# Kernel optimization log

Hardware: AMD Instinct MI355X
Metric: run time of the kernel (lower is better)

The kernel has to match this reference:

```python
import jax, jax.numpy as jnp
import numpy as np

DIM, HEADS = 1536, 12
HD = DIM // HEADS            # 128 head dim
C = HD // 2                  # 64 complex (pair) dim
C0 = C - 2 * (C // 3)        # 22 (temporal axis)
C1 = C // 3                  # 21 (each spatial axis)
MAX_POS = 1024
F_, H_, W_ = 9, 22, 22
SEQ = F_ * H_ * W_           # 4356
NCLASS = 2
EPS = 1e-6


def _rope_tables():
    # Wan rope_params: theta = 10000, per-axis half-dims C0, C1, C1.
    def ang(half):
        inv = 1.0 / (10000.0 ** (np.arange(0, 2 * half, 2) / (2 * half)))
        return np.outer(np.arange(MAX_POS), inv)
    a = np.concatenate([ang(C0), ang(C1), ang(C1)], axis=1)  # [MAX_POS, C]
    return jnp.asarray(np.cos(a), jnp.float32), jnp.asarray(np.sin(a), jnp.float32)


def setup_inputs() -> dict:
    key = jax.random.key(0)
    ks = jax.random.split(key, 6)
    s = 1.0 / np.sqrt(DIM)
    def lin(k):
        k1, k2 = jax.random.split(k)
        return (jax.random.uniform(k1, (DIM, DIM), jnp.float32, -s, s),
                jax.random.uniform(k2, (DIM,), jnp.float32, -s, s))
    Wq, bq = lin(ks[0]); Wk, bk = lin(ks[1]); Wv, bv = lin(ks[2]); Wo, bo = lin(ks[3])
    fc, fs = _rope_tables()
    masks = (jax.random.uniform(ks[4], (NCLASS, H_ * W_)) < 0.5).astype(jnp.float32)
    x = jax.random.normal(ks[5], (1, SEQ, DIM), jnp.float32)
    return {"x": x, "Wq": Wq, "bq": bq, "Wk": Wk, "bk": bk, "Wv": Wv, "bv": bv,
            "Wo": Wo, "bo": bo, "gq": jnp.ones((DIM,), jnp.float32),
            "gk": jnp.ones((DIM,), jnp.float32), "freqs_cos": fc, "freqs_sin": fs,
            "ref_target_masks": masks, "f": F_, "h": H_, "w": W_}


def _rmsnorm(x, g):
    return x * jax.lax.rsqrt(jnp.mean(x * x, axis=-1, keepdims=True) + EPS) * g


def _grid_cs(tab, f, h, w):
    # per-position (f,h,w) rope table -> [f*h*w, C]
    p0 = jnp.broadcast_to(tab[:f, None, None, :C0], (f, h, w, C0))
    p1 = jnp.broadcast_to(tab[None, :h, None, C0:C0 + C1], (f, h, w, C1))
    p2 = jnp.broadcast_to(tab[None, None, :w, C0 + C1:], (f, h, w, C1))
    return jnp.concatenate([p0, p1, p2], axis=-1).reshape(f * h * w, C)


def _rope(x, cos, sin):
    # x: [b,s,n,d]; pairs are interleaved along d (view_as_complex semantics)
    b, s, n, d = x.shape
    xr = x.reshape(b, s, n, d // 2, 2)
    a, bi = xr[..., 0], xr[..., 1]
    cos = cos[None, :, None, :]
    sin = sin[None, :, None, :]
    out = jnp.stack([a * cos - bi * sin, a * sin + bi * cos], axis=-1)
    return out.reshape(b, s, n, d)


def reference(x, Wq, bq, Wk, bk, Wv, bv, Wo, bo, gq, gk, freqs_cos, freqs_sin,
              ref_target_masks, f, h, w):
    b, s, _ = x.shape
    n, d = HEADS, HD
    q = _rmsnorm(x @ Wq.T + bq, gq).reshape(b, s, n, d)
    k = _rmsnorm(x @ Wk.T + bk, gk).reshape(b, s, n, d)
    v = (x @ Wv.T + bv).reshape(b, s, n, d)
    cos = _grid_cs(freqs_cos, f, h, w)
    sin = _grid_cs(freqs_sin, f, h, w)
    q = _rope(q, cos, sin)
    k = _rope(k, cos, sin)
    scale = 1.0 / np.sqrt(d).astype(np.float32)
    # full (window_size == (-1,-1)) attention; seq_lens == s so k_lens mask is identity
    scores = jnp.einsum('bsnd,btnd->bnst', q, k) * scale
    p = jax.nn.softmax(scores, axis=-1)
    o = jnp.einsum('bnst,btnd->bsnd', p, v).reshape(b, s, n * d)
    out = o @ Wo.T + bo
    # aux attention map vs reference-frame keys (first h*w spatial tokens), no-grad path
    xs = h * w
    ref_k = k[:, :xs]
    s2 = jnp.einsum('bsnd,btnd->bnst', q * scale, ref_k)
    p2 = jax.nn.softmax(s2, axis=-1)                       # [b,n,s,xs]
    m = ref_target_masks                                   # [c,xs]
    maps = jnp.einsum('bnst,ct->cbns', p2, m) / jnp.sum(m, axis=-1)[:, None, None, None]
    attn_map = maps.mean(axis=2).reshape(-1, s)            # mean over heads -> [c*b, s]
    return out, attn_map
```

## Files before the change

kernel.cpp:

```cpp
#include <hip/hip_runtime.h>
#include <hip/hip_bf16.h>
#include <math.h>

constexpr int SEQ   = 4356;
constexpr int DIM   = 1536;
constexpr int HEADS = 12;
constexpr int HD    = 128;
constexpr int CH    = 64;
constexpr int C0c   = 22;
constexpr int C1c   = 21;
constexpr int WWc   = 22;
constexpr int HHWW  = 484;
constexpr int XS    = 484;
constexpr int KVB   = 32;
constexpr int NT    = (SEQ + KVB - 1) / KVB;
constexpr int SEQP  = 4416;
constexpr int VP    = 40;
constexpr size_t SD = (size_t)SEQ * DIM;

typedef float f32x4 __attribute__((ext_vector_type(4)));
typedef short bf16x8 __attribute__((ext_vector_type(8)));
typedef short bf16x4 __attribute__((ext_vector_type(4)));

__device__ inline unsigned short f2bf(float f) {
  union { float f; unsigned u; } x; x.f = f;
  return (unsigned short)((x.u + 0x7FFFu + ((x.u >> 16) & 1u)) >> 16);
}

#define GLD16(g, l)                                                                        \
  __builtin_amdgcn_global_load_lds((const __attribute__((address_space(1))) unsigned*)    \
                                       (const void*)(g),                                  \
                                   (__attribute__((address_space(3))) unsigned*)(void*)(l),\
                                   16, 0, 0)

__global__ __launch_bounds__(256) void prep_kernel(const float* __restrict__ mask,
                                                   float* __restrict__ amap,
                                                   float* __restrict__ cnt,
                                                   float4* __restrict__ msk4) {
  int t = threadIdx.x;
  for (int i = t; i < 2 * SEQ; i += 256) amap[i] = 0.f;
  for (int i = t; i < 512; i += 256) {
    float4 v;
    v.x = (i < XS) ? mask[i] : 0.f;
    v.y = (i < XS) ? mask[XS + i] : 0.f;
    v.z = (i < XS) ? 1.f : 0.f;
    v.w = 0.f;
    msk4[i] = v;
  }
  float c0 = 0.f, c1 = 0.f;
  for (int i = t; i < XS; i += 256) { c0 += mask[i]; c1 += mask[XS + i]; }
  __shared__ float red0[256];
  __shared__ float red1[256];
  red0[t] = c0; red1[t] = c1;
  __syncthreads();
  for (int off = 128; off > 0; off >>= 1) {
    if (t < off) { red0[t] += red0[t + off]; red1[t] += red1[t + off]; }
    __syncthreads();
  }
  if (t == 0) { cnt[0] = red0[0]; cnt[1] = red1[0]; }
}

__global__ __launch_bounds__(256) void padzero(unsigned short* __restrict__ vt) {
  const int pad = SEQP - SEQ;
  const int total = DIM * pad;
  for (int i = blockIdx.x * 256 + threadIdx.x; i < total; i += gridDim.x * 256) {
    const int d = i / pad, c = i - d * pad;
    vt[(size_t)d * SEQP + SEQ + c] = 0;
  }
}

__global__ __launch_bounds__(256) void to_bf16(const float* __restrict__ in,
                                               unsigned short* __restrict__ out, int n4) {
  for (int i = blockIdx.x * 256 + threadIdx.x; i < n4; i += gridDim.x * 256) {
    const float4 v = ((const float4*)in)[i];
    ushort4 o;
    o.x = f2bf(v.x); o.y = f2bf(v.y); o.z = f2bf(v.z); o.w = f2bf(v.w);
    ((ushort4*)out)[i] = o;
  }
}

__global__ __launch_bounds__(256) void to_bf16_w(const float* __restrict__ W0, const float* __restrict__ W1,
                                                 const float* __restrict__ W2, const float* __restrict__ W3,
                                                 unsigned short* __restrict__ o0, unsigned short* __restrict__ o1,
                                                 unsigned short* __restrict__ o2, unsigned short* __restrict__ o3,
                                                 int n4) {
  const int z = blockIdx.z;
  const float* in = (z == 0) ? W0 : (z == 1) ? W1 : (z == 2) ? W2 : W3;
  unsigned short* out = (z == 0) ? o0 : (z == 1) ? o1 : (z == 2) ? o2 : o3;
  for (int i = blockIdx.x * 256 + threadIdx.x; i < n4; i += gridDim.x * 256) {
    const float4 v = ((const float4*)in)[i];
    ushort4 o;
    o.x = f2bf(v.x); o.y = f2bf(v.y); o.z = f2bf(v.z); o.w = f2bf(v.w);
    ((ushort4*)out)[i] = o;
  }
}

__global__ __launch_bounds__(256) void gemm_qkv(const unsigned short* __restrict__ A,
                                                const unsigned short* __restrict__ B0,
                                                const unsigned short* __restrict__ B1,
                                                const unsigned short* __restrict__ B2,
                                                const float* __restrict__ bq,
                                                const float* __restrict__ bk,
                                                const float* __restrict__ bv,
                                                float* __restrict__ o0,
                                                float* __restrict__ o1,
                                                unsigned short* __restrict__ vtout,
                                                int M) {
  __shared__ unsigned short As[128 * 64];
  __shared__ unsigned short Bs[128 * 64];
  const int z = blockIdx.z;
  const unsigned short* B = (z == 0) ? B0 : (z == 1) ? B1 : B2;
  const float* bias = (z == 0) ? bq : (z == 1) ? bk : bv;
  const int t    = threadIdx.x;
  const int lane = t & 63;
  const int w    = t >> 6;
  const int wr   = w >> 1, wc = w & 1;
  const int bm = blockIdx.x * 128, bn = blockIdx.y * 128;
  const int lq = lane & 15, lg = lane >> 4;
  f32x4 acc[4][4] = {};
  for (int k0 = 0; k0 < DIM; k0 += 64) {
#pragma unroll
    for (int i = 0; i < 4; ++i) {
      const int idx = i * 256 + t;
      const int row = idx >> 3;
      const int c8  = (idx & 7) * 8;
      const int ga  = min(bm + row, M - 1);
      GLD16(A + (size_t)ga * DIM + k0 + c8, As + idx * 8);
      const int gb  = bn + row;
      GLD16(B + (size_t)gb * DIM + k0 + c8, Bs + idx * 8);
    }
    __syncthreads();
#pragma unroll
    for (int kk = 0; kk < 2; ++kk) {
      bf16x8 af[4], bf[4];
#pragma unroll
      for (int m = 0; m < 4; ++m)
        af[m] = *(const bf16x8*)(As + (wr * 64 + m * 16 + lq) * 64 + kk * 32 + lg * 8);
#pragma unroll
      for (int n = 0; n < 4; ++n)
        bf[n] = *(const bf16x8*)(Bs + (wc * 64 + n * 16 + lq) * 64 + kk * 32 + lg * 8);
#pragma unroll
      for (int m = 0; m < 4; ++m)
#pragma unroll
        for (int n = 0; n < 4; ++n)
          acc[m][n] = __builtin_amdgcn_mfma_f32_16x16x32_bf16(af[m], bf[n], acc[m][n], 0, 0, 0);
    }
    __syncthreads();
  }
#pragma unroll
  for (int n = 0; n < 4; ++n) {
    const int col = bn + wc * 64 + n * 16 + lq;
    const float bv2 = bias[col];
#pragma unroll
    for (int m = 0; m < 4; ++m) {
      const int rm = bm + wr * 64 + m * 16 + lg * 4;
      if (z < 2) {
        float* C = (z == 0) ? o0 : o1;
#pragma unroll
        for (int r = 0; r < 4; ++r) {
          const int row = rm + r;
          if (row < M) C[(size_t)row * DIM + col] = acc[m][n][r] + bv2;
        }
      } else {
        if (rm < M) {
          bf16x4 o;
#pragma unroll
          for (int r = 0; r < 4; ++r) o[r] = (short)f2bf(acc[m][n][r] + bv2);
          *(bf16x4*)(vtout + (size_t)col * SEQP + rm) = o;
        }
      }
    }
  }
}

__global__ __launch_bounds__(256) void gemm_mfma(const unsigned short* __restrict__ A,
                                                 const unsigned short* __restrict__ B,
                                                 const float* __restrict__ bias,
                                                 float* __restrict__ C, int M) {
  __shared__ unsigned short As[128 * 64];
  __shared__ unsigned short Bs[128 * 64];
  const int t    = threadIdx.x;
  const int lane = t & 63;
  const int w    = t >> 6;
  const int wr   = w >> 1, wc = w & 1;
  const int bm = blockIdx.x * 128, bn = blockIdx.y * 128;
  const int lq = lane & 15, lg = lane >> 4;
  f32x4 acc[4][4] = {};
  for (int k0 = 0; k0 < DIM; k0 += 64) {
#pragma unroll
    for (int i = 0; i < 4; ++i) {
      const int idx = i * 256 + t;
      const int row = idx >> 3;
      const int c8  = (idx & 7) * 8;
      const int ga  = min(bm + row, M - 1);
      GLD16(A + (size_t)ga * DIM + k0 + c8, As + idx * 8);
      const int gb  = bn + row;
      GLD16(B + (size_t)gb * DIM + k0 + c8, Bs + idx * 8);
    }
    __syncthreads();
#pragma unroll
    for (int kk = 0; kk < 2; ++kk) {
      bf16x8 af[4], bf[4];
#pragma unroll
      for (int m = 0; m < 4; ++m)
        af[m] = *(const bf16x8*)(As + (wr * 64 + m * 16 + lq) * 64 + kk * 32 + lg * 8);
#pragma unroll
      for (int n = 0; n < 4; ++n)
        bf[n] = *(const bf16x8*)(Bs + (wc * 64 + n * 16 + lq) * 64 + kk * 32 + lg * 8);
#pragma unroll
      for (int m = 0; m < 4; ++m)
#pragma unroll
        for (int n = 0; n < 4; ++n)
          acc[m][n] = __builtin_amdgcn_mfma_f32_16x16x32_bf16(af[m], bf[n], acc[m][n], 0, 0, 0);
    }
    __syncthreads();
  }
#pragma unroll
  for (int n = 0; n < 4; ++n) {
    const int col = bn + wc * 64 + n * 16 + lq;
    const float bv = bias[col];
#pragma unroll
    for (int m = 0; m < 4; ++m) {
      const int rm = bm + wr * 64 + m * 16 + lg * 4;
#pragma unroll
      for (int r = 0; r < 4; ++r) {
        const int row = rm + r;
        if (row < M) C[(size_t)row * DIM + col] = acc[m][n][r] + bv;
      }
    }
  }
}

__global__ __launch_bounds__(256) void rms_rope2(const float* __restrict__ qy,
                                                 const float* __restrict__ ky,
                                                 const float* __restrict__ gq,
                                                 const float* __restrict__ gk,
                                                 const float* __restrict__ fcos,
                                                 const float* __restrict__ fsin,
                                                 unsigned short* __restrict__ qout,
                                                 unsigned short* __restrict__ kout) {
  const int z = blockIdx.y;
  const float* y = z ? ky : qy;
  const float* g = z ? gk : gq;
  unsigned short* outb = z ? kout : qout;
  const float scale = z ? 1.0f : 0.08838834764831845f;
  const int s = blockIdx.x;
  const float* row = y + (size_t)s * DIM;
  const int t = threadIdx.x;
  float ss = 0.f;
  for (int i = t; i < DIM / 4; i += 256) {
    const float4 v = ((const float4*)row)[i];
    ss += v.x * v.x + v.y * v.y + v.z * v.z + v.w * v.w;
  }
#pragma unroll
  for (int off = 1; off < 64; off <<= 1) ss += __shfl_xor(ss, off);
  __shared__ float wred[4];
  if ((t & 63) == 0) wred[t >> 6] = ss;
  __syncthreads();
  const float tot = wred[0] + wred[1] + wred[2] + wred[3];
  const float rs = rsqrtf(tot * (1.0f / DIM) + 1e-6f);
  const int fi  = s / HHWW;
  const int rem = s - fi * HHWW;
  const int hi  = rem / WWc;
  const int wi  = rem - hi * WWc;
  for (int p = t; p < DIM / 2; p += 256) {
    const int head = p >> 6;
    const int c    = p & 63;
    const int idx  = head * HD + 2 * c;
    const int trow = (c < C0c) ? fi : ((c < C0c + C1c) ? hi : wi);
    const float co = fcos[trow * CH + c];
    const float si = fsin[trow * CH + c];
    const float a  = row[idx] * rs * g[idx];
    const float b  = row[idx + 1] * rs * g[idx + 1];
    ushort2 pr;
    pr.x = f2bf((a * co - b * si) * scale);
    pr.y = f2bf((a * si + b * co) * scale);
    *(ushort2*)(outb + (size_t)s * DIM + idx) = pr;
  }
}

#define TILE_BODY(KB_, MAP_, LAST_, PRE_)                                               \
  {                                                                                     \
    const int kb_ = (KB_);                                                              \
    f32x4 sacc[2] = {};                                                                 \
    _Pragma("unroll")                                                                   \
    for (int kbi = 0; kbi < 2; ++kbi) {                                                 \
      const int krow = kbi * 16 + lq;                                                   \
      _Pragma("unroll")                                                                 \
      for (int c = 0; c < 4; ++c) {                                                     \
        const bf16x8 kf = *(const bf16x8*)((char*)Ks + krow * 256 +                     \
                            (((c * 4 + lg) ^ (krow & 7)) * 16));                        \
        sacc[kbi] = __builtin_amdgcn_mfma_f32_16x16x32_bf16(kf, qf[c], sacc[kbi], 0, 0, 0); \
      }                                                                                 \
    }                                                                                   \
    if (PRE_) {                                                                         \
      const int kbn = kb_ + KVB;                                                        \
      _Pragma("unroll")                                                                 \
      for (int j = 0; j < 2; ++j) {                                                     \
        const int ck = t + j * 256;                                                     \
        const int kr = ck >> 4, ks2 = ck & 15;                                          \
        stK[j] = *(const bf16x8*)(kh + (size_t)min(kbn + kr, SEQ - 1) * DIM + ks2 * 8); \
        const int vd = ck >> 2, vs2 = ck & 3;                                           \
        stV[j] = *(const bf16x8*)(vh + (size_t)vd * SEQP + kbn + vs2 * 8);              \
      }                                                                                 \
    }                                                                                   \
    float sv[8];                                                                        \
    float mt = -1e30f;                                                                  \
    _Pragma("unroll")                                                                   \
    for (int i = 0; i < 8; ++i) {                                                       \
      float v = sacc[i >> 2][i & 3];                                                    \
      if (LAST_) {                                                                      \
        const int key = kb_ + (i >> 2) * 16 + lg * 4 + (i & 3);                         \
        if (key >= SEQ) v = -1e30f;                                                     \
      }                                                                                 \
      sv[i] = v;                                                                        \
      mt = fmaxf(mt, v);                                                                \
    }                                                                                   \
    mt = fmaxf(mt, __shfl_xor(mt, 16));                                                 \
    mt = fmaxf(mt, __shfl_xor(mt, 32));                                                 \
    const bool need = __any(mt > m_run + 8.f);                                          \
    if (need) {                                                                         \
      const float m_new = fmaxf(m_run, mt);                                             \
      const float alpha = __expf(m_run - m_new);                                        \
      m_run = m_new;                                                                    \
      l_run *= alpha;                                                                   \
      _Pragma("unroll")                                                                 \
      for (int db = 0; db < 8; ++db) {                                                  \
        acc[db][0] *= alpha; acc[db][1] *= alpha;                                       \
        acc[db][2] *= alpha; acc[db][3] *= alpha;                                       \
      }                                                                                 \
      if (MAP_) { d2 *= alpha; n0 *= alpha; n1 *= alpha; }                              \
    }                                                                                   \
    float ps = 0.f;                                                                     \
    _Pragma("unroll")                                                                   \
    for (int i = 0; i < 8; ++i) { sv[i] = __expf(sv[i] - m_run); ps += sv[i]; }         \
    ps += __shfl_xor(ps, 16);                                                           \
    ps += __shfl_xor(ps, 32);                                                           \
    l_run += ps;                                                                        \
    if (MAP_) {                                                                         \
      _Pragma("unroll")                                                                 \
      for (int i = 0; i < 8; ++i) {                                                     \
        const int key = kb_ + (i >> 2) * 16 + lg * 4 + (i & 3);                         \
        const float4 mv = Msk[key];                                                     \
        n0 = fmaf(sv[i], mv.x, n0);                                                     \
        n1 = fmaf(sv[i], mv.y, n1);                                                     \
        d2 = fmaf(sv[i], mv.z, d2);                                                     \
      }                                                                                 \
    }                                                                                   \
    _Pragma("unroll")                                                                   \
    for (int kbi = 0; kbi < 2; ++kbi) {                                                 \
      unsigned r0, r1;                                                                  \
      asm("v_cvt_pk_bf16_f32 %0, %1, %2" : "=v"(r0) : "v"(sv[kbi * 4 + 0]), "v"(sv[kbi * 4 + 1])); \
      asm("v_cvt_pk_bf16_f32 %0, %1, %2" : "=v"(r1) : "v"(sv[kbi * 4 + 2]), "v"(sv[kbi * 4 + 3])); \
      uint2 pw; pw.x = r0; pw.y = r1;                                                   \
      *(uint2*)&P[lq][kbi * 16 + lg * 4] = pw;                                          \
    }                                                                                   \
    {                                                                                   \
      const bf16x8 pf = *(const bf16x8*)&P[lq][lg * 8];                                 \
      _Pragma("unroll")                                                                 \
      for (int db = 0; db < 8; ++db) {                                                  \
        const bf16x8 vf = *(const bf16x8*)(Vs + (db * 16 + lq) * VP + lg * 8);          \
        acc[db] = __builtin_amdgcn_mfma_f32_16x16x32_bf16(vf, pf, acc[db], 0, 0, 0);    \
      }                                                                                 \
    }                                                                                   \
    if (PRE_) {                                                                         \
      __syncthreads();                                                                  \
      _Pragma("unroll")                                                                 \
      for (int j = 0; j < 2; ++j) {                                                     \
        const int ck = t + j * 256;                                                     \
        const int kr = ck >> 4, ks2 = ck & 15;                                          \
        *(bf16x8*)((char*)Ks + kr * 256 + ((ks2 ^ (kr & 7)) * 16)) = stK[j];            \
        const int vd = ck >> 2, vs2 = ck & 3;                                           \
        *(bf16x8*)(Vs + vd * VP + vs2 * 8) = stV[j];                                    \
      }                                                                                 \
      __syncthreads();                                                                  \
    }                                                                                   \
  }

__global__ __launch_bounds__(256, 4) void flash_mfma(const unsigned short* __restrict__ qbuf,
                                                     const unsigned short* __restrict__ kbuf,
                                                     const unsigned short* __restrict__ vt,
                                                     const float4* __restrict__ msk4,
                                                     const float* __restrict__ cnt,
                                                     unsigned short* __restrict__ ob,
                                                     float* __restrict__ amap) {
  const int h    = blockIdx.y;
  const int t    = threadIdx.x;
  const int w    = t >> 6;
  const int lane = t & 63;
  const int lq   = lane & 15, lg = lane >> 4;
  const int qbase = blockIdx.x * 64 + w * 16;

  __shared__ __align__(16) unsigned short Ks[KVB * 128];
  __shared__ __align__(16) unsigned short Vs[128 * VP];
  __shared__ __align__(16) unsigned short Plds[4][16][72];
  __shared__ float4 Msk[512];
  unsigned short (*P)[72] = Plds[w];

  const unsigned short* kh = kbuf + h * HD;
  const unsigned short* vh = vt + (size_t)(h * HD) * SEQP;

  for (int i = t; i < 512; i += 256) Msk[i] = msk4[i];

  const int qsrc = min(qbase + lq, SEQ - 1);
  bf16x8 qf[4];
#pragma unroll
  for (int c = 0; c < 4; ++c)
    qf[c] = *(const bf16x8*)(qbuf + (size_t)qsrc * DIM + h * HD + c * 32 + lg * 8);

  f32x4 acc[8] = {};
  float m_run = -1e30f, l_run = 0.f;
  float d2 = 0.f, n0 = 0.f, n1 = 0.f;

  bf16x8 stK[2], stV[2];
#pragma unroll
  for (int j = 0; j < 2; ++j) {
    const int ck = t + j * 256;
    const int kr = ck >> 4, ks2 = ck & 15;
    stK[j] = *(const bf16x8*)(kh + (size_t)min(kr, SEQ - 1) * DIM + ks2 * 8);
    const int vd = ck >> 2, vs2 = ck & 3;
    stV[j] = *(const bf16x8*)(vh + (size_t)vd * SEQP + vs2 * 8);
  }
#pragma unroll
  for (int j = 0; j < 2; ++j) {
    const int ck = t + j * 256;
    const int kr = ck >> 4, ks2 = ck & 15;
    *(bf16x8*)((char*)Ks + kr * 256 + ((ks2 ^ (kr & 7)) * 16)) = stK[j];
    const int vd = ck >> 2, vs2 = ck & 3;
    *(bf16x8*)(Vs + vd * VP + vs2 * 8) = stV[j];
  }
  __syncthreads();

  for (int tile = 0; tile < 16; ++tile)         TILE_BODY(tile * KVB, true,  false, true);
  for (int tile = 16; tile < NT - 1; ++tile)    TILE_BODY(tile * KVB, false, false, true);
  TILE_BODY((NT - 1) * KVB, false, true, false);

  const int qrow = qbase + lq;
  if (qrow < SEQ) {
    const float inv = 1.f / l_run;
#pragma unroll
    for (int db = 0; db < 8; ++db) {
      bf16x4 o;
#pragma unroll
      for (int r = 0; r < 4; ++r) o[r] = (short)f2bf(acc[db][r] * inv);
      *(bf16x4*)(ob + (size_t)qrow * DIM + h * HD + db * 16 + lg * 4) = o;
    }
  }
  d2 += __shfl_xor(d2, 16); d2 += __shfl_xor(d2, 32);
  n0 += __shfl_xor(n0, 16); n0 += __shfl_xor(n0, 32);
  n1 += __shfl_xor(n1, 16); n1 += __shfl_xor(n1, 32);
  if (lane < 16 && qrow < SEQ) {
    const float invd = 1.f / (d2 * (float)HEADS);
    atomicAdd(&amap[qrow],       n0 * invd / cnt[0]);
    atomicAdd(&amap[SEQ + qrow], n1 * invd / cnt[1]);
  }
}

extern "C" void kernel_launch(void* const* d_in, const int* in_sizes, int n_in,
                              void* d_out, int out_size, void* d_ws, size_t ws_size,
                              hipStream_t stream) {
  const float* x    = (const float*)d_in[0];
  const float* Wq   = (const float*)d_in[1];
  const float* bq   = (const float*)d_in[2];
  const float* Wk   = (const float*)d_in[3];
  const float* bk   = (const float*)d_in[4];
  const float* Wv   = (const float*)d_in[5];
  const float* bv   = (const float*)d_in[6];
  const float* Wo   = (const float*)d_in[7];
  const float* bo   = (const float*)d_in[8];
  const float* gq   = (const float*)d_in[9];
  const float* gk   = (const float*)d_in[10];
  const float* fc   = (const float*)d_in[11];
  const float* fs   = (const float*)d_in[12];
  const float* mask = (const float*)d_in[13];

  float* out  = (float*)d_out;
  float* amap = out + SD;
  float* f32a = out;

  float* f32b        = (float*)d_ws;
  unsigned short* xb = (unsigned short*)(f32b + SD);
  unsigned short* qb = xb + SD;
  unsigned short* kb = qb + SD;
  unsigned short* vt = kb + SD;
  unsigned short* wqb = vt + (size_t)DIM * SEQP;
  unsigned short* wkb = wqb + (size_t)DIM * DIM;
  unsigned short* wvb = wkb + (size_t)DIM * DIM;
  unsigned short* wob = wvb + (size_t)DIM * DIM;
  float4* msk4 = (float4*)(wob + (size_t)DIM * DIM);
  float* cnt  = (float*)(msk4 + 512);
  unsigned short* ob = (unsigned short*)f32b;

  prep_kernel<<<1, 256, 0, stream>>>(mask, amap, cnt, msk4);
  padzero<<<64, 256, 0, stream>>>(vt);
  to_bf16<<<2048, 256, 0, stream>>>(x, xb, (int)(SD / 4));
  constexpr int W4 = DIM * DIM / 4;
  to_bf16_w<<<dim3(512, 1, 4), 256, 0, stream>>>(Wq, Wk, Wv, Wo, wqb, wkb, wvb, wob, W4);

  const dim3 gg((SEQ + 127) / 128, DIM / 128, 3);
  gemm_qkv<<<gg, 256, 0, stream>>>(xb, wqb, wkb, wvb, bq, bk, bv, f32a, f32b, vt, SEQ);

  rms_rope2<<<dim3(SEQ, 2), 256, 0, stream>>>(f32a, f32b, gq, gk, fc, fs, qb, kb);

  const dim3 fg((SEQ + 63) / 64, HEADS);
  flash_mfma<<<fg, 256, 0, stream>>>(qb, kb, vt, msk4, cnt, ob, amap);

  const dim3 go((SEQ + 127) / 128, DIM / 128);
  gemm_mfma<<<go, 256, 0, stream>>>(ob, wob, bo, out, SEQ);
}
```

Before: 467.2 us.

## Process two query sub-tiles per wave with double-buffered direct-to-LDS K/V loads

Each wave of the flash attention kernel now handles 32 query rows (two 16-row sub-tiles) rather than 16, so every K and V fragment read from LDS feeds two MFMAs and the block covers 128 queries. K/V tiles are double-buffered in LDS and filled asynchronously with global_load_lds using XOR-swizzled addresses, which drops the register staging copy and one of the two barriers per tile. The cost is roughly double the accumulator registers (launch bounds lowered to 3 waves per SIMD) and half as many blocks in the grid, which could hurt occupancy and tail balance.

```diff
diff --git a/kernel.cpp b/kernel.cpp
--- a/kernel.cpp
+++ b/kernel.cpp
@@ -15,7 +15,6 @@
 constexpr int KVB   = 32;
 constexpr int NT    = (SEQ + KVB - 1) / KVB;
 constexpr int SEQP  = 4416;
-constexpr int VP    = 40;
 constexpr size_t SD = (size_t)SEQ * DIM;
 
 typedef float f32x4 __attribute__((ext_vector_type(4)));
@@ -279,105 +278,103 @@
   }
 }
 
-#define TILE_BODY(KB_, MAP_, LAST_, PRE_)                                               \
-  {                                                                                     \
-    const int kb_ = (KB_);                                                              \
-    f32x4 sacc[2] = {};                                                                 \
-    _Pragma("unroll")                                                                   \
-    for (int kbi = 0; kbi < 2; ++kbi) {                                                 \
-      const int krow = kbi * 16 + lq;                                                   \
-      _Pragma("unroll")                                                                 \
-      for (int c = 0; c < 4; ++c) {                                                     \
-        const bf16x8 kf = *(const bf16x8*)((char*)Ks + krow * 256 +                     \
-                            (((c * 4 + lg) ^ (krow & 7)) * 16));                        \
-        sacc[kbi] = __builtin_amdgcn_mfma_f32_16x16x32_bf16(kf, qf[c], sacc[kbi], 0, 0, 0); \
-      }                                                                                 \
-    }                                                                                   \
-    if (PRE_) {                                                                         \
-      const int kbn = kb_ + KVB;                                                        \
-      _Pragma("unroll")                                                                 \
-      for (int j = 0; j < 2; ++j) {                                                     \
-        const int ck = t + j * 256;                                                     \
-        const int kr = ck >> 4, ks2 = ck & 15;                                          \
-        stK[j] = *(const bf16x8*)(kh + (size_t)min(kbn + kr, SEQ - 1) * DIM + ks2 * 8); \
-        const int vd = ck >> 2, vs2 = ck & 3;                                           \
-        stV[j] = *(const bf16x8*)(vh + (size_t)vd * SEQP + kbn + vs2 * 8);              \
-      }                                                                                 \
-    }                                                                                   \
-    float sv[8];                                                                        \
-    float mt = -1e30f;                                                                  \
-    _Pragma("unroll")                                                                   \
-    for (int i = 0; i < 8; ++i) {                                                       \
-      float v = sacc[i >> 2][i & 3];                                                    \
-      if (LAST_) {                                                                      \
-        const int key = kb_ + (i >> 2) * 16 + lg * 4 + (i & 3);                         \
-        if (key >= SEQ) v = -1e30f;                                                     \
-      }                                                                                 \
-      sv[i] = v;                                                                        \
-      mt = fmaxf(mt, v);                                                                \
-    }                                                                                   \
-    mt = fmaxf(mt, __shfl_xor(mt, 16));                                                 \
-    mt = fmaxf(mt, __shfl_xor(mt, 32));                                                 \
-    const bool need = __any(mt > m_run + 8.f);                                          \
-    if (need) {                                                                         \
-      const float m_new = fmaxf(m_run, mt);                                             \
-      const float alpha = __expf(m_run - m_new);                                        \
-      m_run = m_new;                                                                    \
-      l_run *= alpha;                                                                   \
-      _Pragma("unroll")                                                                 \
-      for (int db = 0; db < 8; ++db) {                                                  \
-        acc[db][0] *= alpha; acc[db][1] *= alpha;                                       \
-        acc[db][2] *= alpha; acc[db][3] *= alpha;                                       \
-      }                                                                                 \
-      if (MAP_) { d2 *= alpha; n0 *= alpha; n1 *= alpha; }                              \
-    }                                                                                   \
-    float ps = 0.f;                                                                     \
-    _Pragma("unroll")                                                                   \
-    for (int i = 0; i < 8; ++i) { sv[i] = __expf(sv[i] - m_run); ps += sv[i]; }         \
-    ps += __shfl_xor(ps, 16);                                                           \
-    ps += __shfl_xor(ps, 32);                                                           \
-    l_run += ps;                                                                        \
-    if (MAP_) {                                                                         \
-      _Pragma("unroll")                                                                 \
-      for (int i = 0; i < 8; ++i) {                                                     \
-        const int key = kb_ + (i >> 2) * 16 + lg * 4 + (i & 3);                         \
-        const float4 mv = Msk[key];                                                     \
-        n0 = fmaf(sv[i], mv.x, n0);                                                     \
-        n1 = fmaf(sv[i], mv.y, n1);                                                     \
-        d2 = fmaf(sv[i], mv.z, d2);                                                     \
-      }                                                                                 \
-    }                                                                                   \
-    _Pragma("unroll")                                                                   \
-    for (int kbi = 0; kbi < 2; ++kbi) {                                                 \
-      unsigned r0, r1;                                                                  \
-      asm("v_cvt_pk_bf16_f32 %0, %1, %2" : "=v"(r0) : "v"(sv[kbi * 4 + 0]), "v"(sv[kbi * 4 + 1])); \
-      asm("v_cvt_pk_bf16_f32 %0, %1, %2" : "=v"(r1) : "v"(sv[kbi * 4 + 2]), "v"(sv[kbi * 4 + 3])); \
-      uint2 pw; pw.x = r0; pw.y = r1;                                                   \
-      *(uint2*)&P[lq][kbi * 16 + lg * 4] = pw;                                          \
-    }                                                                                   \
-    {                                                                                   \
-      const bf16x8 pf = *(const bf16x8*)&P[lq][lg * 8];                                 \
-      _Pragma("unroll")                                                                 \
-      for (int db = 0; db < 8; ++db) {                                                  \
-        const bf16x8 vf = *(const bf16x8*)(Vs + (db * 16 + lq) * VP + lg * 8);          \
-        acc[db] = __builtin_amdgcn_mfma_f32_16x16x32_bf16(vf, pf, acc[db], 0, 0, 0);    \
-      }                                                                                 \
-    }                                                                                   \
-    if (PRE_) {                                                                         \
-      __syncthreads();                                                                  \
-      _Pragma("unroll")                                                                 \
-      for (int j = 0; j < 2; ++j) {                                                     \
-        const int ck = t + j * 256;                                                     \
-        const int kr = ck >> 4, ks2 = ck & 15;                                          \
-        *(bf16x8*)((char*)Ks + kr * 256 + ((ks2 ^ (kr & 7)) * 16)) = stK[j];            \
-        const int vd = ck >> 2, vs2 = ck & 3;                                           \
-        *(bf16x8*)(Vs + vd * VP + vs2 * 8) = stV[j];                                    \
-      }                                                                                 \
-      __syncthreads();                                                                  \
-    }                                                                                   \
-  }
-
-__global__ __launch_bounds__(256, 4) void flash_mfma(const unsigned short* __restrict__ qbuf,
+#define SOFT_QS(QS, SACC, ACC, MAP_, LAST_, KBV)                                           \
+  {                                                                                        \
+    float sv[8]; float mt = -1e30f;                                                        \
+    _Pragma("unroll")                                                                      \
+    for (int i = 0; i < 8; ++i) {                                                          \
+      float v = SACC[i >> 2][i & 3];                                                       \
+      if (LAST_) { const int key = (KBV) + (i >> 2) * 16 + lg * 4 + (i & 3);               \
+                   if (key >= SEQ) v = -1e30f; }                                           \
+      sv[i] = v; mt = fmaxf(mt, v);                                                        \
+    }                                                                                      \
+    mt = fmaxf(mt, __shfl_xor(mt, 16));                                                    \
+    mt = fmaxf(mt, __shfl_xor(mt, 32));                                                    \
+    if (__any(mt > m_run[QS] + 8.f)) {                                                     \
+      const float m_new = fmaxf(m_run[QS], mt);                                            \
+      const float alpha = __expf(m_run[QS] - m_new);                                       \
+      m_run[QS] = m_new; l_run[QS] *= alpha;                                               \
+      _Pragma("unroll")                                                                    \
+      for (int db = 0; db < 8; ++db) {                                                     \
+        ACC[db][0] *= alpha; ACC[db][1] *= alpha;                                          \
+        ACC[db][2] *= alpha; ACC[db][3] *= alpha;                                          \
+      }                                                                                    \
+      if (MAP_) { d2[QS] *= alpha; n0[QS] *= alpha; n1[QS] *= alpha; }                     \
+    }                                                                                      \
+    float ps = 0.f;                                                                        \
+    _Pragma("unroll")                                                                      \
+    for (int i = 0; i < 8; ++i) { sv[i] = __expf(sv[i] - m_run[QS]); ps += sv[i]; }        \
+    ps += __shfl_xor(ps, 16); ps += __shfl_xor(ps, 32);                                    \
+    l_run[QS] += ps;                                                                       \
+    if (MAP_) {                                                                            \
+      _Pragma("unroll")                                                                    \
+      for (int i = 0; i < 8; ++i) {                                                        \
+        const int key = (KBV) + (i >> 2) * 16 + lg * 4 + (i & 3);                          \
+        const float4 mv = Msk[key];                                                        \
+        n0[QS] = fmaf(sv[i], mv.x, n0[QS]);                                                \
+        n1[QS] = fmaf(sv[i], mv.y, n1[QS]);                                                \
+        d2[QS] = fmaf(sv[i], mv.z, d2[QS]);                                                \
+      }                                                                                    \
+    }                                                                                      \
+    _Pragma("unroll")                                                                      \
+    for (int kbi = 0; kbi < 2; ++kbi) {                                                    \
+      unsigned r0, r1;                                                                     \
+      asm("v_cvt_pk_bf16_f32 %0, %1, %2" : "=v"(r0) : "v"(sv[kbi*4+0]), "v"(sv[kbi*4+1])); \
+      asm("v_cvt_pk_bf16_f32 %0, %1, %2" : "=v"(r1) : "v"(sv[kbi*4+2]), "v"(sv[kbi*4+3])); \
+      uint2 pw; pw.x = r0; pw.y = r1;                                                      \
+      *(uint2*)&Pw[QS][lq][kbi * 16 + lg * 4] = pw;                                        \
+    }                                                                                      \
+  }
+
+#define TILE_BODY(KB_, MAP_, LAST_, PRE_)                                                  \
+  {                                                                                        \
+    const int kb_ = (KB_);                                                                 \
+    const int cur_ = (kb_ >> 5) & 1;                                                       \
+    const unsigned short* Kc = Ks[cur_];                                                   \
+    const unsigned short* Vc = Vs[cur_];                                                   \
+    if (PRE_) {                                                                            \
+      unsigned short* Kn = Ks[cur_ ^ 1];                                                   \
+      unsigned short* Vn = Vs[cur_ ^ 1];                                                   \
+      const int kbn = kb_ + KVB;                                                           \
+      _Pragma("unroll")                                                                    \
+      for (int j = 0; j < 2; ++j) {                                                        \
+        const int ck = t + j * 256;                                                        \
+        const int kr = ck >> 4, ksl = ck & 15;                                             \
+        GLD16(kh + (size_t)min(kbn + kr, SEQ - 1) * DIM + ((ksl ^ (kr & 7)) * 8),          \
+              Kn + ck * 8);                                                                \
+        const int vd = ck >> 2, vsl = ck & 3;                                              \
+        GLD16(vh + (size_t)vd * SEQP + kbn + ((vsl ^ ((vd >> 1) & 3)) * 8),                \
+              Vn + ck * 8);                                                                \
+      }                                                                                    \
+    }                                                                                      \
+    f32x4 sacc0[2] = {}, sacc1[2] = {};                                                    \
+    _Pragma("unroll")                                                                      \
+    for (int kbi = 0; kbi < 2; ++kbi) {                                                    \
+      const int krow = kbi * 16 + lq;                                                      \
+      _Pragma("unroll")                                                                    \
+      for (int c = 0; c < 4; ++c) {                                                        \
+        const bf16x8 kf = *(const bf16x8*)(Kc + (krow * 16 + ((c * 4 + lg) ^ (krow & 7))) * 8); \
+        sacc0[kbi] = __builtin_amdgcn_mfma_f32_16x16x32_bf16(kf, qf0[c], sacc0[kbi], 0, 0, 0);  \
+        sacc1[kbi] = __builtin_amdgcn_mfma_f32_16x16x32_bf16(kf, qf1[c], sacc1[kbi], 0, 0, 0);  \
+      }                                                                                    \
+    }                                                                                      \
+    SOFT_QS(0, sacc0, acc0, MAP_, LAST_, kb_)                                              \
+    SOFT_QS(1, sacc1, acc1, MAP_, LAST_, kb_)                                              \
+    {                                                                                      \
+      const bf16x8 pf0 = *(const bf16x8*)&Pw[0][lq][lg * 8];                               \
+      const bf16x8 pf1 = *(const bf16x8*)&Pw[1][lq][lg * 8];                               \
+      _Pragma("unroll")                                                                    \
+      for (int db = 0; db < 8; ++db) {                                                     \
+        const int vd = db * 16 + lq;                                                       \
+        const bf16x8 vf = *(const bf16x8*)(Vc + (vd * 4 + (lg ^ ((vd >> 1) & 3))) * 8);    \
+        acc0[db] = __builtin_amdgcn_mfma_f32_16x16x32_bf16(vf, pf0, acc0[db], 0, 0, 0);    \
+        acc1[db] = __builtin_amdgcn_mfma_f32_16x16x32_bf16(vf, pf1, acc1[db], 0, 0, 0);    \
+      }                                                                                    \
+    }                                                                                      \
+    if (PRE_) __syncthreads();                                                             \
+  }
+
+__global__ __launch_bounds__(256, 3) void flash_mfma(const unsigned short* __restrict__ qbuf,
                                                      const unsigned short* __restrict__ kbuf,
                                                      const unsigned short* __restrict__ vt,
                                                      const float4* __restrict__ msk4,
@@ -389,45 +386,39 @@
   const int w    = t >> 6;
   const int lane = t & 63;
   const int lq   = lane & 15, lg = lane >> 4;
-  const int qbase = blockIdx.x * 64 + w * 16;
-
-  __shared__ __align__(16) unsigned short Ks[KVB * 128];
-  __shared__ __align__(16) unsigned short Vs[128 * VP];
-  __shared__ __align__(16) unsigned short Plds[4][16][72];
+  const int qbase = blockIdx.x * 128 + w * 32;
+
+  __shared__ __align__(16) unsigned short Ks[2][KVB * 128];
+  __shared__ __align__(16) unsigned short Vs[2][128 * KVB];
+  __shared__ __align__(16) unsigned short Plds[4][2][16][40];
   __shared__ float4 Msk[512];
-  unsigned short (*P)[72] = Plds[w];
+  unsigned short (*Pw)[16][40] = Plds[w];
 
   const unsigned short* kh = kbuf + h * HD;
   const unsigned short* vh = vt + (size_t)(h * HD) * SEQP;
 
   for (int i = t; i < 512; i += 256) Msk[i] = msk4[i];
 
-  const int qsrc = min(qbase + lq, SEQ - 1);
-  bf16x8 qf[4];
-#pragma unroll
-  for (int c = 0; c < 4; ++c)
-    qf[c] = *(const bf16x8*)(qbuf + (size_t)qsrc * DIM + h * HD + c * 32 + lg * 8);
-
-  f32x4 acc[8] = {};
-  float m_run = -1e30f, l_run = 0.f;
-  float d2 = 0.f, n0 = 0.f, n1 = 0.f;
-
-  bf16x8 stK[2], stV[2];
+  const int qsrc0 = min(qbase + lq, SEQ - 1);
+  const int qsrc1 = min(qbase + 16 + lq, SEQ - 1);
+  bf16x8 qf0[4], qf1[4];
+#pragma unroll
+  for (int c = 0; c < 4; ++c) {
+    qf0[c] = *(const bf16x8*)(qbuf + (size_t)qsrc0 * DIM + h * HD + c * 32 + lg * 8);
+    qf1[c] = *(const bf16x8*)(qbuf + (size_t)qsrc1 * DIM + h * HD + c * 32 + lg * 8);
+  }
+
+  f32x4 acc0[8] = {}, acc1[8] = {};
+  float m_run[2] = {-1e30f, -1e30f}, l_run[2] = {0.f, 0.f};
+  float d2[2] = {0.f, 0.f}, n0[2] = {0.f, 0.f}, n1[2] = {0.f, 0.f};
+
 #pragma unroll
   for (int j = 0; j < 2; ++j) {
     const int ck = t + j * 256;
-    const int kr = ck >> 4, ks2 = ck & 15;
-    stK[j] = *(const bf16x8*)(kh + (size_t)min(kr, SEQ - 1) * DIM + ks2 * 8);
-    const int vd = ck >> 2, vs2 = ck & 3;
-    stV[j] = *(const bf16x8*)(vh + (size_t)vd * SEQP + vs2 * 8);
-  }
-#pragma unroll
-  for (int j = 0; j < 2; ++j) {
-    const int ck = t + j * 256;
-    const int kr = ck >> 4, ks2 = ck & 15;
-    *(bf16x8*)((char*)Ks + kr * 256 + ((ks2 ^ (kr & 7)) * 16)) = stK[j];
-    const int vd = ck >> 2, vs2 = ck & 3;
-    *(bf16x8*)(Vs + vd * VP + vs2 * 8) = stV[j];
+    const int kr = ck >> 4, ksl = ck & 15;
+    GLD16(kh + (size_t)min(kr, SEQ - 1) * DIM + ((ksl ^ (kr & 7)) * 8), Ks[0] + ck * 8);
+    const int vd = ck >> 2, vsl = ck & 3;
+    GLD16(vh + (size_t)vd * SEQP + ((vsl ^ ((vd >> 1) & 3)) * 8), Vs[0] + ck * 8);
   }
   __syncthreads();
 
@@ -435,24 +426,44 @@
   for (int tile = 16; tile < NT - 1; ++tile)    TILE_BODY(tile * KVB, false, false, true);
   TILE_BODY((NT - 1) * KVB, false, true, false);
 
-  const int qrow = qbase + lq;
-  if (qrow < SEQ) {
-    const float inv = 1.f / l_run;
-#pragma unroll
-    for (int db = 0; db < 8; ++db) {
-      bf16x4 o;
-#pragma unroll
-      for (int r = 0; r < 4; ++r) o[r] = (short)f2bf(acc[db][r] * inv);
-      *(bf16x4*)(ob + (size_t)qrow * DIM + h * HD + db * 16 + lg * 4) = o;
-    }
-  }
-  d2 += __shfl_xor(d2, 16); d2 += __shfl_xor(d2, 32);
-  n0 += __shfl_xor(n0, 16); n0 += __shfl_xor(n0, 32);
-  n1 += __shfl_xor(n1, 16); n1 += __shfl_xor(n1, 32);
-  if (lane < 16 && qrow < SEQ) {
-    const float invd = 1.f / (d2 * (float)HEADS);
-    atomicAdd(&amap[qrow],       n0 * invd / cnt[0]);
-    atomicAdd(&amap[SEQ + qrow], n1 * invd / cnt[1]);
+  {
+    const int qrow = qbase + lq;
+    if (qrow < SEQ) {
+      const float inv = 1.f / l_run[0];
+#pragma unroll
+      for (int db = 0; db < 8; ++db) {
+        bf16x4 o;
+#pragma unroll
+        for (int r = 0; r < 4; ++r) o[r] = (short)f2bf(acc0[db][r] * inv);
+        *(bf16x4*)(ob + (size_t)qrow * DIM + h * HD + db * 16 + lg * 4) = o;
+      }
+    }
+  }
+  {
+    const int qrow = qbase + 16 + lq;
+    if (qrow < SEQ) {
+      const float inv = 1.f / l_run[1];
+#pragma unroll
+      for (int db = 0; db < 8; ++db) {
+        bf16x4 o;
+#pragma unroll
+        for (int r = 0; r < 4; ++r) o[r] = (short)f2bf(acc1[db][r] * inv);
+        *(bf16x4*)(ob + (size_t)qrow * DIM + h * HD + db * 16 + lg * 4) = o;
+      }
+    }
+  }
+#pragma unroll
+  for (int qs = 0; qs < 2; ++qs) {
+    float dd = d2[qs], a0 = n0[qs], a1 = n1[qs];
+    dd += __shfl_xor(dd, 16); dd += __shfl_xor(dd, 32);
+    a0 += __shfl_xor(a0, 16); a0 += __shfl_xor(a0, 32);
+    a1 += __shfl_xor(a1, 16); a1 += __shfl_xor(a1, 32);
+    const int qrow = qbase + qs * 16 + lq;
+    if (lane < 16 && qrow < SEQ) {
+      const float invd = 1.f / (dd * (float)HEADS);
+      atomicAdd(&amap[qrow],       a0 * invd / cnt[0]);
+      atomicAdd(&amap[SEQ + qrow], a1 * invd / cnt[1]);
+    }
   }
 }
 
@@ -502,7 +513,7 @@
 
   rms_rope2<<<dim3(SEQ, 2), 256, 0, stream>>>(f32a, f32b, gq, gk, fc, fs, qb, kb);
 
-  const dim3 fg((SEQ + 63) / 64, HEADS);
+  const dim3 fg((SEQ + 127) / 128, HEADS);
   flash_mfma<<<fg, 256, 0, stream>>>(qb, kb, vt, msk4, cnt, ob, amap);
 
   const dim3 go((SEQ + 127) / 128, DIM / 128);
```

After: 445.9 us. -4.6%, faster.
